# Kernel optimization log

Hardware: AMD Instinct MI355X
Metric: run time of the kernel (lower is better)

Reference implementation:

```python
import jax, jax.numpy as jnp
import numpy as np

N = 6000          # num nodes (max_nodes)
E = 192000        # num edges
NTYPES = 100
NCLUST = 4        # hardcoded num_nodes=4 in diff_pool_net.__init__
OUT = 16
BN_EPS = 1e-5

PARAM_SHAPES = {
    'emb_w': (NTYPES, 64),
    # gnn1_pool: GNN(64, 64, 4, lin=True); DenseSAGEConv: lin_rel (no bias) + lin_root (bias)
    'pw1r': (64, 64), 'pw1l': (64, 64), 'pb1': (64,),
    'pw2r': (64, 64), 'pw2l': (64, 64), 'pb2': (64,),
    'pw3r': (NCLUST, 64), 'pw3l': (NCLUST, 64), 'pb3': (NCLUST,),
    'plin_w': (NCLUST, 2 * 64 + NCLUST), 'plin_b': (NCLUST,),
    # gnn1_embed: GNN(64, 64, 64, lin=False)
    'ew1r': (64, 64), 'ew1l': (64, 64), 'eb1': (64,),
    'ew2r': (64, 64), 'ew2l': (64, 64), 'eb2': (64,),
    'ew3r': (64, 64), 'ew3l': (64, 64), 'eb3': (64,),
    'lin1_w': (64, 192), 'lin1_b': (64,),
    'lin2_w': (OUT, 64), 'lin2_b': (OUT,),
    'embl_w': (32, 192), 'embl_b': (32,),
    'lin3_w': (OUT, 32 + OUT), 'lin3_b': (OUT,),
}


def _lin(x, w, b=None):
    y = x @ w.T
    return y if b is None else y + b


def _sage(x, adj, wr, wl, b):
    # DenseSAGEConv: mean-aggregate over dense adj, then lin_rel(agg) + lin_root(x)
    agg = jnp.matmul(adj, x)
    deg = jnp.clip(jnp.sum(adj, axis=-1, keepdims=True), 1.0, None)
    return _lin(agg / deg, wr) + _lin(x, wl, b)


def _bn(x):
    # training-mode BatchNorm1d with default gamma=1, beta=0 (biased variance)
    c = x.shape[-1]
    xf = x.reshape(-1, c)
    m = jnp.mean(xf, axis=0)
    v = jnp.var(xf, axis=0)
    return ((xf - m) * jax.lax.rsqrt(v + BN_EPS)).reshape(x.shape)


def _gnn(x, adj, wr1, wl1, b1, wr2, wl2, b2, wr3, wl3, b3, lw=None, lb=None):
    x1 = _bn(jax.nn.relu(_sage(x, adj, wr1, wl1, b1)))
    x2 = _bn(jax.nn.relu(_sage(x1, adj, wr2, wl2, b2)))
    x3 = _bn(jax.nn.relu(_sage(x2, adj, wr3, wl3, b3)))
    xc = jnp.concatenate([x1, x2, x3], axis=-1)
    if lw is not None:
        xc = jax.nn.relu(_lin(xc, lw, lb))
    return xc


def _forward(p, edge_index, node_types):
    # to_dense_adj: scatter-add edges into a dense [1, N, N] adjacency
    adj = jnp.zeros((N, N), jnp.float32).at[edge_index[0], edge_index[1]].add(1.0)[None]
    x = p['emb_w'][node_types][None]                      # [1, N, 64]
    s = _gnn(x, adj, p['pw1r'], p['pw1l'], p['pb1'],
             p['pw2r'], p['pw2l'], p['pb2'],
             p['pw3r'], p['pw3l'], p['pb3'],
             p['plin_w'], p['plin_b'])                    # [1, N, 4]
    xe = _gnn(x, adj, p['ew1r'], p['ew1l'], p['eb1'],
              p['ew2r'], p['ew2l'], p['eb2'],
              p['ew3r'], p['ew3l'], p['eb3'])             # [1, N, 192]
    x_embed = _lin(xe, p['embl_w'], p['embl_b'])          # [1, N, 32]
    # dense_diff_pool pooled features: softmax(S)^T @ X (pooled adj/losses are unused downstream)
    ssm = jax.nn.softmax(s, axis=-1)
    s_x = jnp.einsum('bnk,bnc->bkc', ssm, xe)             # [1, 4, 192]
    s_x = jax.nn.relu(_lin(s_x, p['lin1_w'], p['lin1_b']))
    s_x = _lin(s_x, p['lin2_w'], p['lin2_b'])             # [1, 4, OUT]
    # one_hot=True branch: per-node gather of its cluster row (vectorized form of the python loop)
    idx = jnp.argmax(s, axis=-1)                          # [1, N]
    res = jnp.take(s_x[0], idx[0], axis=0)[None]          # [1, N, OUT]
    return _lin(jnp.concatenate([x_embed, res], axis=-1), p['lin3_w'], p['lin3_b'])


def setup_inputs() -> dict:
    key = jax.random.key(0)
    ks = jax.random.split(key, len(PARAM_SHAPES) + 2)
    inp = {n: jax.random.normal(k, shp, jnp.float32) * 0.1
           for (n, shp), k in zip(PARAM_SHAPES.items(), ks)}
    inp['edge_index'] = jax.random.randint(ks[-2], (2, E), 0, N)
    inp['node_types'] = jax.random.randint(ks[-1], (N,), 0, NTYPES)
    return inp


def reference(edge_index, node_types, emb_w, pw1r, pw1l, pb1, pw2r, pw2l, pb2,
              pw3r, pw3l, pb3, plin_w, plin_b, ew1r, ew1l, eb1, ew2r, ew2l, eb2,
              ew3r, ew3l, eb3, lin1_w, lin1_b, lin2_w, lin2_b, embl_w, embl_b,
              lin3_w, lin3_b):
    args = locals()
    p = {k: args[k] for k in PARAM_SHAPES}
    return _forward(p, edge_index, node_types)
```

## Files before the change

kernel.cpp:

```cpp
#include <hip/hip_runtime.h>
#include <hip/hip_bf16.h>

#define NN 6000
#define EE 192000

#define W_DEG     0
#define W_CUR     6000
#define W_STATS   12000
#define W_SXACC   12768
#define W_ZEND    13536
#define W_FLAG    13536
#define W_ROWPTR  13540
#define W_COL     19544
#define W_X0      211544
#define W_ZP1     595544
#define W_ZP2     979544
#define W_ZP3     1363544
#define W_ZE1     1387544
#define W_ZE2     1771544
#define W_ZE3     2155544
#define W_S       2539544
#define W_SX2     2563544
#define W_PAR     2563608

struct PtrTab {
  const void* src[29];
  int off[29];
  int cnt[29];
};

__device__ __forceinline__ float bf2f(unsigned short h) {
  return __uint_as_float(((unsigned)h) << 16);
}
__device__ __forceinline__ int rfl(int x) { return __builtin_amdgcn_readfirstlane(x); }

__global__ void k_detect(const void* emb, int* flag) {
  __shared__ int bad;
  if (threadIdx.x == 0) bad = 0;
  __syncthreads();
  const unsigned short* p = (const unsigned short*)emb;
  float v0 = bf2f(p[threadIdx.x]);
  float v1 = bf2f(p[threadIdx.x + 256]);
  if (!(fabsf(v0) <= 100.f) || !(fabsf(v1) <= 100.f)) bad = 1;
  __syncthreads();
  if (threadIdx.x == 0) flag[0] = bad ? 0 : 1;
}

__global__ void k_convert(PtrTab tab, float* base, const int* flag) {
  int b = blockIdx.x;
  const void* s = tab.src[b];
  float* d = base + tab.off[b];
  int n = tab.cnt[b];
  bool bf = (flag[0] == 1);
  if (bf) {
    const unsigned short* sp = (const unsigned short*)s;
    for (int i = threadIdx.x; i < n; i += 256) d[i] = bf2f(sp[i]);
  } else {
    const float* sp = (const float*)s;
    for (int i = threadIdx.x; i < n; i += 256) d[i] = sp[i];
  }
}

__global__ void k_deg(const int* __restrict__ ei, int* __restrict__ deg) {
  int e = blockIdx.x * 256 + threadIdx.x;
  if (e < EE) atomicAdd(&deg[ei[e]], 1);
}

__global__ void k_scan(const int* __restrict__ deg, int* __restrict__ rowptr) {
  __shared__ int part[1024];
  int t = threadIdx.x;
  int base = t * 6;
  int loc[6]; int s = 0;
#pragma unroll
  for (int j = 0; j < 6; ++j) { int i = base + j; int v = (i < NN) ? deg[i] : 0; loc[j] = s; s += v; }
  part[t] = s;
  __syncthreads();
  for (int off = 1; off < 1024; off <<= 1) {
    int v = part[t];
    int add = (t >= off) ? part[t - off] : 0;
    __syncthreads();
    part[t] = v + add;
    __syncthreads();
  }
  int pre = (t == 0) ? 0 : part[t - 1];
#pragma unroll
  for (int j = 0; j < 6; ++j) { int i = base + j; if (i <= NN) rowptr[i] = pre + loc[j]; }
}

__global__ void k_scatter(const int* __restrict__ ei, const int* __restrict__ rowptr,
                          int* __restrict__ cur, int* __restrict__ col) {
  int e = blockIdx.x * 256 + threadIdx.x;
  if (e < EE) {
    int s = ei[e], d = ei[EE + e];
    int pos = atomicAdd(&cur[s], 1);
    col[rowptr[s] + pos] = d;
  }
}

__global__ void k_emb(const float* __restrict__ emb, const int* __restrict__ nt, float* __restrict__ x0) {
  int t = blockIdx.x * 256 + threadIdx.x;
  int i = t >> 4, q = t & 15;
  *(float4*)&x0[i * 64 + q * 4] = *(const float4*)&emb[nt[i] * 64 + q * 4];
}

template <int OUT, bool HS>
__device__ __forceinline__ void sage_body(
    const float* __restrict__ in_z, const float* __restrict__ in_stats,
    const float* __restrict__ wr, const float* __restrict__ wl, const float* __restrict__ bias,
    const int* __restrict__ rowptr, const int* __restrict__ col,
    float* __restrict__ out_z, float* __restrict__ out_stats,
    int vb, int total_waves,
    float* __restrict__ wrT, float* __restrict__ wlT, float* __restrict__ bs,
    float (* __restrict__ vec)[2][64], float (* __restrict__ red)[2][64]) {
  int tid = threadIdx.x, lane = tid & 63, wv = tid >> 6;

  for (int i = tid; i < 64 * OUT; i += 256) {
    int f = i >> 6, k = i & 63;
    wrT[k * (OUT + 1) + f] = wr[i];
    wlT[k * (OUT + 1) + f] = wl[i];
  }
  if (tid < OUT) bs[tid] = bias[tid];

  float m = 0.f, r = 1.f;
  if (HS) {
    float s = in_stats[lane], q = in_stats[64 + lane];
    m = s * (1.f / NN);
    r = rsqrtf(q * (1.f / NN) - m * m + 1e-5f);
  }
  __syncthreads();

  float accs = 0.f, accq = 0.f;
  int ol = lane & (OUT - 1);
  int wave_id = vb * 4 + wv;
  for (int n = wave_id; n < NN; n += total_waves) {
    float x = (in_z[n * 64 + lane] - m) * r;
    int rs = rfl(rowptr[n]), re = rfl(rowptr[n + 1]);
    int cnt = re - rs;
    float sz = 0.f;
    for (int base = rs; base < re; base += 64) {
      int ci = base + lane;
      int colv = col[ci < re ? ci : (re - 1)];
      int full = re - base; if (full > 64) full = 64;
      int ng8 = (full + 7) >> 3;
      for (int g = 0; g < ng8; ++g) {
        int e0 = g * 8;
#pragma unroll
        for (int u = 0; u < 8; ++u) {
          int j = __builtin_amdgcn_readlane(colv, e0 + u);
          float v = in_z[j * 64 + lane];
          sz += (e0 + u < full) ? v : 0.f;
        }
      }
    }
    float fc = (float)cnt;
    float inv = 1.f / (float)(cnt > 0 ? cnt : 1);
    float a = (sz - fc * m) * r * inv;
    vec[wv][0][lane] = a;
    vec[wv][1][lane] = x;
    float y = bs[ol];
    const float* va = &vec[wv][0][0];
    const float* vx = &vec[wv][1][0];
#pragma unroll
    for (int kk = 0; kk < 16; ++kk) {
      const float4 a4 = *(const float4*)(va + kk * 4);
      const float4 x4 = *(const float4*)(vx + kk * 4);
      int k0 = kk * 4;
      y += a4.x * wrT[(k0 + 0) * (OUT + 1) + ol] + x4.x * wlT[(k0 + 0) * (OUT + 1) + ol];
      y += a4.y * wrT[(k0 + 1) * (OUT + 1) + ol] + x4.y * wlT[(k0 + 1) * (OUT + 1) + ol];
      y += a4.z * wrT[(k0 + 2) * (OUT + 1) + ol] + x4.z * wlT[(k0 + 2) * (OUT + 1) + ol];
      y += a4.w * wrT[(k0 + 3) * (OUT + 1) + ol] + x4.w * wlT[(k0 + 3) * (OUT + 1) + ol];
    }
    float z = fmaxf(y, 0.f);
    if (lane < OUT) {
      out_z[n * OUT + lane] = z;
      accs += z; accq += z * z;
    }
  }
  if (lane < OUT) { red[wv][0][lane] = accs; red[wv][1][lane] = accq; }
  __syncthreads();
  if (tid < OUT) {
    float s = red[0][0][tid] + red[1][0][tid] + red[2][0][tid] + red[3][0][tid];
    float q = red[0][1][tid] + red[1][1][tid] + red[2][1][tid] + red[3][1][tid];
    atomicAdd(&out_stats[tid], s);
    atomicAdd(&out_stats[64 + tid], q);
  }
}

template <int OUTA, int OUTB, bool HS>
__global__ __launch_bounds__(256, 4) void k_dual(
    const float* __restrict__ inA, const float* __restrict__ stA,
    const float* __restrict__ wrA, const float* __restrict__ wlA, const float* __restrict__ bA,
    float* __restrict__ outA, float* __restrict__ ostA,
    const float* __restrict__ inB, const float* __restrict__ stB,
    const float* __restrict__ wrB, const float* __restrict__ wlB, const float* __restrict__ bB,
    float* __restrict__ outB, float* __restrict__ ostB,
    const int* __restrict__ rowptr, const int* __restrict__ col, int G) {
  __shared__ float wrT[64 * 65];
  __shared__ float wlT[64 * 65];
  __shared__ float bs[64];
  __shared__ float vec[4][2][64];
  __shared__ float red[4][2][64];
  int bx = (int)blockIdx.x;
  int hi = (bx >> 2) & 1;
  int vb = (bx >> 3) * 4 + (bx & 3);
  if (hi == 0)
    sage_body<OUTA, HS>(inA, stA, wrA, wlA, bA, rowptr, col, outA, ostA,
                        vb, G * 4, wrT, wlT, bs, vec, red);
  else
    sage_body<OUTB, HS>(inB, stB, wrB, wlB, bB, rowptr, col, outB, ostB,
                        vb, G * 4, wrT, wlT, bs, vec, red);
}

__global__ __launch_bounds__(256) void k_pool(
    const float* __restrict__ zp1, const float* __restrict__ zp2, const float* __restrict__ zp3,
    const float* __restrict__ sp1, const float* __restrict__ sp2, const float* __restrict__ sp3,
    const float* __restrict__ ze1, const float* __restrict__ ze2, const float* __restrict__ ze3,
    const float* __restrict__ se1, const float* __restrict__ se2, const float* __restrict__ se3,
    const float* __restrict__ plw, const float* __restrict__ plb,
    float* __restrict__ s_out, float* __restrict__ sx_acc) {
  __shared__ float red[4][12][64];
  int tid = threadIdx.x, lane = tid & 63, wv = tid >> 6;

  float mp1 = sp1[lane] * (1.f / NN); float rp1 = rsqrtf(sp1[64 + lane] * (1.f / NN) - mp1 * mp1 + 1e-5f);
  float mp2 = sp2[lane] * (1.f / NN); float rp2 = rsqrtf(sp2[64 + lane] * (1.f / NN) - mp2 * mp2 + 1e-5f);
  float mp3 = 0.f, rp3 = 1.f;
  if (lane < 4) { mp3 = sp3[lane] * (1.f / NN); rp3 = rsqrtf(sp3[64 + lane] * (1.f / NN) - mp3 * mp3 + 1e-5f); }
  float me1 = se1[lane] * (1.f / NN); float re1 = rsqrtf(se1[64 + lane] * (1.f / NN) - me1 * me1 + 1e-5f);
  float me2 = se2[lane] * (1.f / NN); float re2 = rsqrtf(se2[64 + lane] * (1.f / NN) - me2 * me2 + 1e-5f);
  float me3 = se3[lane] * (1.f / NN); float re3 = rsqrtf(se3[64 + lane] * (1.f / NN) - me3 * me3 + 1e-5f);

  float w0a = plw[0 * 132 + lane], w0b = plw[0 * 132 + 64 + lane], w0c = (lane < 4) ? plw[0 * 132 + 128 + lane] : 0.f;
  float w1a = plw[1 * 132 + lane], w1b = plw[1 * 132 + 64 + lane], w1c = (lane < 4) ? plw[1 * 132 + 128 + lane] : 0.f;
  float w2a = plw[2 * 132 + lane], w2b = plw[2 * 132 + 64 + lane], w2c = (lane < 4) ? plw[2 * 132 + 128 + lane] : 0.f;
  float w3a = plw[3 * 132 + lane], w3b = plw[3 * 132 + 64 + lane], w3c = (lane < 4) ? plw[3 * 132 + 128 + lane] : 0.f;
  float pb0 = plb[0], pb1v = plb[1], pb2v = plb[2], pb3v = plb[3];

  float acc[12];
#pragma unroll
  for (int u = 0; u < 12; ++u) acc[u] = 0.f;

  int wave_id = blockIdx.x * 4 + wv;
  for (int n = wave_id; n < NN; n += 1500) {
    float a = (zp1[n * 64 + lane] - mp1) * rp1;
    float b = (zp2[n * 64 + lane] - mp2) * rp2;
    float c = (lane < 4) ? ((zp3[n * 4 + lane] - mp3) * rp3) : 0.f;
    float p0 = a * w0a + b * w0b + c * w0c;
    float p1 = a * w1a + b * w1b + c * w1c;
    float p2 = a * w2a + b * w2b + c * w2c;
    float p3 = a * w3a + b * w3b + c * w3c;
#pragma unroll
    for (int off = 1; off < 64; off <<= 1) {
      p0 += __shfl_xor(p0, off);
      p1 += __shfl_xor(p1, off);
      p2 += __shfl_xor(p2, off);
      p3 += __shfl_xor(p3, off);
    }
    float s0 = fmaxf(p0 + pb0, 0.f), s1 = fmaxf(p1 + pb1v, 0.f);
    float s2 = fmaxf(p2 + pb2v, 0.f), s3 = fmaxf(p3 + pb3v, 0.f);
    if (lane < 4) {
      float sv = (lane == 0) ? s0 : (lane == 1) ? s1 : (lane == 2) ? s2 : s3;
      s_out[n * 4 + lane] = sv;
    }
    float mx = fmaxf(fmaxf(s0, s1), fmaxf(s2, s3));
    float e0 = __expf(s0 - mx), e1 = __expf(s1 - mx), e2 = __expf(s2 - mx), e3 = __expf(s3 - mx);
    float inv = 1.f / (e0 + e1 + e2 + e3);
    e0 *= inv; e1 *= inv; e2 *= inv; e3 *= inv;
    float x1 = (ze1[n * 64 + lane] - me1) * re1;
    float x2 = (ze2[n * 64 + lane] - me2) * re2;
    float x3 = (ze3[n * 64 + lane] - me3) * re3;
    acc[0] += e0 * x1; acc[1] += e0 * x2; acc[2] += e0 * x3;
    acc[3] += e1 * x1; acc[4] += e1 * x2; acc[5] += e1 * x3;
    acc[6] += e2 * x1; acc[7] += e2 * x2; acc[8] += e2 * x3;
    acc[9] += e3 * x1; acc[10] += e3 * x2; acc[11] += e3 * x3;
  }
#pragma unroll
  for (int u = 0; u < 12; ++u) red[wv][u][lane] = acc[u];
  __syncthreads();
  for (int u = tid; u < 768; u += 256) {
    int f = u & 63, q = u >> 6;
    float v = red[0][q][f] + red[1][q][f] + red[2][q][f] + red[3][q][f];
    int k = q / 3, slot = q - 3 * k;
    atomicAdd(&sx_acc[k * 192 + slot * 64 + f], v);
  }
}

__global__ void k_mlp(const float* __restrict__ sx, const float* __restrict__ l1w, const float* __restrict__ l1b,
                      const float* __restrict__ l2w, const float* __restrict__ l2b, float* __restrict__ sx2) {
  __shared__ float tl[4][64];
  int tid = threadIdx.x;
  int k = tid >> 6, f = tid & 63;
  float v = l1b[f];
  for (int c = 0; c < 192; ++c) v += sx[k * 192 + c] * l1w[f * 192 + c];
  tl[k][f] = fmaxf(v, 0.f);
  __syncthreads();
  if (tid < 64) {
    int kk = tid >> 4, o = tid & 15;
    float u = l2b[o];
#pragma unroll
    for (int j = 0; j < 64; ++j) u += tl[kk][j] * l2w[o * 64 + j];
    sx2[kk * 16 + o] = u;
  }
}

__global__ __launch_bounds__(256) void k_final(
    const float* __restrict__ ze1, const float* __restrict__ ze2, const float* __restrict__ ze3,
    const float* __restrict__ se1, const float* __restrict__ se2, const float* __restrict__ se3,
    const float* __restrict__ ew, const float* __restrict__ ebv,
    const float* __restrict__ l3w, const float* __restrict__ l3b,
    const float* __restrict__ s_out, const float* __restrict__ sx2,
    const int* __restrict__ flag, void* __restrict__ out) {
  __shared__ float ewT[192 * 33];
  __shared__ float l3T[48 * 17];
  __shared__ float ebs[32], l3bs[16];
  __shared__ float xev[4][192];
  __shared__ float xed[4][32];
  int tid = threadIdx.x, lane = tid & 63, wv = tid >> 6;

  for (int i = tid; i < 6144; i += 256) { int cp = i / 192, c = i - cp * 192; ewT[c * 33 + cp] = ew[i]; }
  for (int i = tid; i < 768; i += 256) { int o = i / 48, j = i - o * 48; l3T[j * 17 + o] = l3w[i]; }
  if (tid < 32) ebs[tid] = ebv[tid];
  if (tid < 16) l3bs[tid] = l3b[tid];

  float me1 = se1[lane] * (1.f / NN); float re1 = rsqrtf(se1[64 + lane] * (1.f / NN) - me1 * me1 + 1e-5f);
  float me2 = se2[lane] * (1.f / NN); float re2 = rsqrtf(se2[64 + lane] * (1.f / NN) - me2 * me2 + 1e-5f);
  float me3 = se3[lane] * (1.f / NN); float re3 = rsqrtf(se3[64 + lane] * (1.f / NN) - me3 * me3 + 1e-5f);
  bool bf = (flag[0] == 1);
  __syncthreads();

  int h = lane >> 5, L = lane & 31;
  int wave_id = blockIdx.x * 4 + wv;
  for (int n = wave_id; n < NN; n += 2048) {
    float x1 = (ze1[n * 64 + lane] - me1) * re1;
    float x2 = (ze2[n * 64 + lane] - me2) * re2;
    float x3 = (ze3[n * 64 + lane] - me3) * re3;
    xev[wv][lane] = x1;
    xev[wv][64 + lane] = x2;
    xev[wv][128 + lane] = x3;
    float v = (h == 0) ? ebs[L] : 0.f;
    int cb = h * 96;
#pragma unroll
    for (int c4 = 0; c4 < 24; ++c4) {
      const float4 xv = *(const float4*)&xev[wv][cb + c4 * 4];
      int c0 = cb + c4 * 4;
      v += xv.x * ewT[(c0 + 0) * 33 + L];
      v += xv.y * ewT[(c0 + 1) * 33 + L];
      v += xv.z * ewT[(c0 + 2) * 33 + L];
      v += xv.w * ewT[(c0 + 3) * 33 + L];
    }
    v += __shfl_xor(v, 32);
    if (h == 0) xed[wv][L] = v;
    if (lane < 16) {
      int idx = 0; float best = s_out[n * 4 + 0];
      float c1 = s_out[n * 4 + 1]; if (c1 > best) { best = c1; idx = 1; }
      float c2 = s_out[n * 4 + 2]; if (c2 > best) { best = c2; idx = 2; }
      float c3 = s_out[n * 4 + 3]; if (c3 > best) { best = c3; idx = 3; }
      float racc = l3bs[lane];
#pragma unroll
      for (int j = 0; j < 32; ++j) racc += xed[wv][j] * l3T[j * 17 + lane];
      const float* sxr = sx2 + idx * 16;
#pragma unroll
      for (int j = 0; j < 16; ++j) racc += sxr[j] * l3T[(32 + j) * 17 + lane];
      if (bf) ((__hip_bfloat16*)out)[n * 16 + lane] = __float2bfloat16(racc);
      else    ((float*)out)[n * 16 + lane] = racc;
    }
  }
}

extern "C" void kernel_launch(void* const* d_in, const int* in_sizes, int n_in,
                              void* d_out, int out_size, void* d_ws, size_t ws_size,
                              hipStream_t stream) {
  float* F = (float*)d_ws;
  int* I = (int*)d_ws;

  static const int pcnt[29] = {6400, 4096, 4096, 64, 4096, 4096, 64, 256, 256, 4, 528, 4,
                               4096, 4096, 64, 4096, 4096, 64, 4096, 4096, 64,
                               12288, 64, 1024, 16, 6144, 32, 768, 16};
  int poff[29];
  { int a = 0; for (int i = 0; i < 29; ++i) { poff[i] = a; a += pcnt[i]; } }

  PtrTab tab;
  for (int i = 0; i < 29; ++i) { tab.src[i] = d_in[i]; tab.off[i] = poff[i]; tab.cnt[i] = pcnt[i]; }

  const int* ei = (const int*)d_in[29];
  const int* nt = (const int*)d_in[30];

  int* deg = I + W_DEG;
  int* cur = I + W_CUR;
  int* rowptr = I + W_ROWPTR;
  int* col = I + W_COL;
  int* flag = I + W_FLAG;
  float* st = F + W_STATS;
  float* sxacc = F + W_SXACC;
  float* x0 = F + W_X0;
  float* zp1 = F + W_ZP1; float* zp2 = F + W_ZP2; float* zp3 = F + W_ZP3;
  float* ze1 = F + W_ZE1; float* ze2 = F + W_ZE2; float* ze3 = F + W_ZE3;
  float* sbuf = F + W_S;
  float* sx2 = F + W_SX2;
  float* P = F + W_PAR;
#define PP(i) (P + poff[i])

  hipMemsetAsync(d_ws, 0, (size_t)W_ZEND * 4, stream);
  k_detect<<<1, 256, 0, stream>>>(d_in[0], flag);
  k_convert<<<29, 256, 0, stream>>>(tab, P, flag);
  k_deg<<<750, 256, 0, stream>>>(ei, deg);
  k_scan<<<1, 1024, 0, stream>>>(deg, rowptr);
  k_scatter<<<750, 256, 0, stream>>>(ei, rowptr, cur, col);
  k_emb<<<375, 256, 0, stream>>>(PP(0), nt, x0);

  k_dual<64, 64, false><<<1024, 256, 0, stream>>>(
      x0, nullptr, PP(1), PP(2), PP(3), zp1, st + 0 * 128,
      x0, nullptr, PP(12), PP(13), PP(14), ze1, st + 3 * 128,
      rowptr, col, 512);
  k_dual<64, 64, true><<<1024, 256, 0, stream>>>(
      zp1, st + 0 * 128, PP(4), PP(5), PP(6), zp2, st + 1 * 128,
      ze1, st + 3 * 128, PP(15), PP(16), PP(17), ze2, st + 4 * 128,
      rowptr, col, 512);
  k_dual<4, 64, true><<<1024, 256, 0, stream>>>(
      zp2, st + 1 * 128, PP(7), PP(8), PP(9), zp3, st + 2 * 128,
      ze2, st + 4 * 128, PP(18), PP(19), PP(20), ze3, st + 5 * 128,
      rowptr, col, 512);

  k_pool<<<375, 256, 0, stream>>>(zp1, zp2, zp3, st + 0 * 128, st + 1 * 128, st + 2 * 128,
                                  ze1, ze2, ze3, st + 3 * 128, st + 4 * 128, st + 5 * 128,
                                  PP(10), PP(11), sbuf, sxacc);
  k_mlp<<<1, 256, 0, stream>>>(sxacc, PP(21), PP(22), PP(23), PP(24), sx2);
  k_final<<<512, 256, 0, stream>>>(ze1, ze2, ze3, st + 3 * 128, st + 4 * 128, st + 5 * 128,
                                   PP(25), PP(26), PP(27), PP(28), sbuf, sx2, flag, d_out);
}
```

Measured before the change: 291.6 us.

## Fuse prelude kernels, fold MLP into final kernel, process two nodes per wave in SAGE

Merges the dtype-detect, parameter-convert, embedding-gather and degree-count kernels into one prelude launch, with every block redoing the cheap detection itself. Folds the tiny cluster MLP into each block of the final kernel so it no longer runs as a separate single-block launch. Changes the SAGE aggregation so each wave handles two nodes at once, interleaving their neighbor gathers to expose more memory-level parallelism. The trade-offs are the MLP being recomputed redundantly in every final block, higher register pressure, and wasted lanes when the two nodes' degrees differ.

```diff
diff --git a/kernel.cpp b/kernel.cpp
--- a/kernel.cpp
+++ b/kernel.cpp
@@ -34,36 +34,50 @@
 }
 __device__ __forceinline__ int rfl(int x) { return __builtin_amdgcn_readfirstlane(x); }
 
-__global__ void k_detect(const void* emb, int* flag) {
-  __shared__ int bad;
-  if (threadIdx.x == 0) bad = 0;
-  __syncthreads();
-  const unsigned short* p = (const unsigned short*)emb;
-  float v0 = bf2f(p[threadIdx.x]);
-  float v1 = bf2f(p[threadIdx.x + 256]);
-  if (!(fabsf(v0) <= 100.f) || !(fabsf(v1) <= 100.f)) bad = 1;
-  __syncthreads();
-  if (threadIdx.x == 0) flag[0] = bad ? 0 : 1;
-}
-
-__global__ void k_convert(PtrTab tab, float* base, const int* flag) {
+__global__ __launch_bounds__(256) void k_prelude(
+    PtrTab tab, float* __restrict__ base,
+    const int* __restrict__ nt, float* __restrict__ x0,
+    const int* __restrict__ ei, int* __restrict__ deg, int* __restrict__ flag) {
+  __shared__ int s_ok;
+  int tid = threadIdx.x;
+  const unsigned short* ep = (const unsigned short*)tab.src[0];
+  if (tid == 0) s_ok = 1;
+  __syncthreads();
+  float v0 = bf2f(ep[tid]), v1 = bf2f(ep[tid + 256]);
+  if (!(fabsf(v0) <= 100.f) || !(fabsf(v1) <= 100.f)) atomicAnd(&s_ok, 0);
+  __syncthreads();
+  bool bf = (s_ok != 0);
   int b = blockIdx.x;
-  const void* s = tab.src[b];
-  float* d = base + tab.off[b];
-  int n = tab.cnt[b];
-  bool bf = (flag[0] == 1);
-  if (bf) {
-    const unsigned short* sp = (const unsigned short*)s;
-    for (int i = threadIdx.x; i < n; i += 256) d[i] = bf2f(sp[i]);
+  if (b == 0 && tid == 0) flag[0] = bf ? 1 : 0;
+
+  if (b < 29) {
+    const void* s = tab.src[b];
+    float* d = base + tab.off[b];
+    int n = tab.cnt[b];
+    if (bf) {
+      const unsigned short* sp = (const unsigned short*)s;
+      for (int i = tid; i < n; i += 256) d[i] = bf2f(sp[i]);
+    } else {
+      const float* sp = (const float*)s;
+      for (int i = tid; i < n; i += 256) d[i] = sp[i];
+    }
+  } else if (b < 404) {
+    int t = (b - 29) * 256 + tid;
+    int i = t >> 4, q = t & 15;
+    int row = nt[i];
+    if (bf) {
+      const unsigned short* sp = (const unsigned short*)tab.src[0] + row * 64 + q * 4;
+      float4 o;
+      o.x = bf2f(sp[0]); o.y = bf2f(sp[1]); o.z = bf2f(sp[2]); o.w = bf2f(sp[3]);
+      *(float4*)&x0[i * 64 + q * 4] = o;
+    } else {
+      *(float4*)&x0[i * 64 + q * 4] =
+          *(const float4*)((const float*)tab.src[0] + row * 64 + q * 4);
+    }
   } else {
-    const float* sp = (const float*)s;
-    for (int i = threadIdx.x; i < n; i += 256) d[i] = sp[i];
-  }
-}
-
-__global__ void k_deg(const int* __restrict__ ei, int* __restrict__ deg) {
-  int e = blockIdx.x * 256 + threadIdx.x;
-  if (e < EE) atomicAdd(&deg[ei[e]], 1);
+    int e = (b - 404) * 256 + tid;
+    if (e < EE) atomicAdd(&deg[ei[e]], 1);
+  }
 }
 
 __global__ void k_scan(const int* __restrict__ deg, int* __restrict__ rowptr) {
@@ -95,12 +109,6 @@
     int pos = atomicAdd(&cur[s], 1);
     col[rowptr[s] + pos] = d;
   }
-}
-
-__global__ void k_emb(const float* __restrict__ emb, const int* __restrict__ nt, float* __restrict__ x0) {
-  int t = blockIdx.x * 256 + threadIdx.x;
-  int i = t >> 4, q = t & 15;
-  *(float4*)&x0[i * 64 + q * 4] = *(const float4*)&emb[nt[i] * 64 + q * 4];
 }
 
 template <int OUT, bool HS>
@@ -111,7 +119,7 @@
     float* __restrict__ out_z, float* __restrict__ out_stats,
     int vb, int total_waves,
     float* __restrict__ wrT, float* __restrict__ wlT, float* __restrict__ bs,
-    float (* __restrict__ vec)[2][64], float (* __restrict__ red)[2][64]) {
+    float (* __restrict__ vec)[4][64], float (* __restrict__ red)[2][64]) {
   int tid = threadIdx.x, lane = tid & 63, wv = tid >> 6;
 
   for (int i = tid; i < 64 * OUT; i += 256) {
@@ -132,48 +140,78 @@
   float accs = 0.f, accq = 0.f;
   int ol = lane & (OUT - 1);
   int wave_id = vb * 4 + wv;
-  for (int n = wave_id; n < NN; n += total_waves) {
-    float x = (in_z[n * 64 + lane] - m) * r;
-    int rs = rfl(rowptr[n]), re = rfl(rowptr[n + 1]);
-    int cnt = re - rs;
-    float sz = 0.f;
-    for (int base = rs; base < re; base += 64) {
-      int ci = base + lane;
-      int colv = col[ci < re ? ci : (re - 1)];
-      int full = re - base; if (full > 64) full = 64;
-      int ng8 = (full + 7) >> 3;
+  int stride2 = 2 * total_waves;
+  for (int n0 = wave_id; n0 < NN; n0 += stride2) {
+    int n1 = n0 + total_waves;
+    bool has1 = n1 < NN;
+    float x0v = (in_z[n0 * 64 + lane] - m) * r;
+    float x1v = has1 ? (in_z[n1 * 64 + lane] - m) * r : 0.f;
+    int rs0 = rfl(rowptr[n0]), re0 = rfl(rowptr[n0 + 1]);
+    int rs1 = rs0, re1 = rs0;
+    if (has1) { rs1 = rfl(rowptr[n1]); re1 = rfl(rowptr[n1 + 1]); }
+    int cnt0 = re0 - rs0, cnt1 = re1 - rs1;
+    float sz0 = 0.f, sz1 = 0.f;
+    int it0 = (cnt0 + 63) >> 6, it1 = (cnt1 + 63) >> 6;
+    int iters = it0 > it1 ? it0 : it1;
+    for (int c = 0; c < iters; ++c) {
+      int b0 = rs0 + (c << 6), b1 = rs1 + (c << 6);
+      int ci0 = b0 + lane, ci1 = b1 + lane;
+      int colv0 = col[(c < it0 && ci0 < re0) ? ci0 : 0];
+      int colv1 = col[(c < it1 && ci1 < re1) ? ci1 : 0];
+      int full0 = re0 - b0; full0 = full0 < 0 ? 0 : (full0 > 64 ? 64 : full0);
+      int full1 = re1 - b1; full1 = full1 < 0 ? 0 : (full1 > 64 ? 64 : full1);
+      int fm = full0 > full1 ? full0 : full1;
+      int ng8 = (fm + 7) >> 3;
       for (int g = 0; g < ng8; ++g) {
         int e0 = g * 8;
 #pragma unroll
         for (int u = 0; u < 8; ++u) {
-          int j = __builtin_amdgcn_readlane(colv, e0 + u);
-          float v = in_z[j * 64 + lane];
-          sz += (e0 + u < full) ? v : 0.f;
+          int j0 = __builtin_amdgcn_readlane(colv0, e0 + u);
+          int j1 = __builtin_amdgcn_readlane(colv1, e0 + u);
+          float v0 = in_z[j0 * 64 + lane];
+          float v1 = in_z[j1 * 64 + lane];
+          sz0 += (e0 + u < full0) ? v0 : 0.f;
+          sz1 += (e0 + u < full1) ? v1 : 0.f;
         }
       }
     }
-    float fc = (float)cnt;
-    float inv = 1.f / (float)(cnt > 0 ? cnt : 1);
-    float a = (sz - fc * m) * r * inv;
-    vec[wv][0][lane] = a;
-    vec[wv][1][lane] = x;
-    float y = bs[ol];
-    const float* va = &vec[wv][0][0];
-    const float* vx = &vec[wv][1][0];
+    float fc0 = (float)cnt0, inv0 = 1.f / (float)(cnt0 > 0 ? cnt0 : 1);
+    float fc1 = (float)cnt1, inv1 = 1.f / (float)(cnt1 > 0 ? cnt1 : 1);
+    float a0 = (sz0 - fc0 * m) * r * inv0;
+    float a1 = (sz1 - fc1 * m) * r * inv1;
+    vec[wv][0][lane] = a0;
+    vec[wv][1][lane] = x0v;
+    vec[wv][2][lane] = a1;
+    vec[wv][3][lane] = x1v;
+    float y0 = bs[ol], y1 = y0;
+    const float* va0 = &vec[wv][0][0];
+    const float* vx0 = &vec[wv][1][0];
+    const float* va1 = &vec[wv][2][0];
+    const float* vx1 = &vec[wv][3][0];
 #pragma unroll
     for (int kk = 0; kk < 16; ++kk) {
-      const float4 a4 = *(const float4*)(va + kk * 4);
-      const float4 x4 = *(const float4*)(vx + kk * 4);
+      const float4 A0 = *(const float4*)(va0 + kk * 4);
+      const float4 X0 = *(const float4*)(vx0 + kk * 4);
+      const float4 A1 = *(const float4*)(va1 + kk * 4);
+      const float4 X1 = *(const float4*)(vx1 + kk * 4);
       int k0 = kk * 4;
-      y += a4.x * wrT[(k0 + 0) * (OUT + 1) + ol] + x4.x * wlT[(k0 + 0) * (OUT + 1) + ol];
-      y += a4.y * wrT[(k0 + 1) * (OUT + 1) + ol] + x4.y * wlT[(k0 + 1) * (OUT + 1) + ol];
-      y += a4.z * wrT[(k0 + 2) * (OUT + 1) + ol] + x4.z * wlT[(k0 + 2) * (OUT + 1) + ol];
-      y += a4.w * wrT[(k0 + 3) * (OUT + 1) + ol] + x4.w * wlT[(k0 + 3) * (OUT + 1) + ol];
-    }
-    float z = fmaxf(y, 0.f);
+      float w_r0 = wrT[(k0 + 0) * (OUT + 1) + ol], w_l0 = wlT[(k0 + 0) * (OUT + 1) + ol];
+      float w_r1 = wrT[(k0 + 1) * (OUT + 1) + ol], w_l1 = wlT[(k0 + 1) * (OUT + 1) + ol];
+      float w_r2 = wrT[(k0 + 2) * (OUT + 1) + ol], w_l2 = wlT[(k0 + 2) * (OUT + 1) + ol];
+      float w_r3 = wrT[(k0 + 3) * (OUT + 1) + ol], w_l3 = wlT[(k0 + 3) * (OUT + 1) + ol];
+      y0 += A0.x * w_r0 + X0.x * w_l0;  y1 += A1.x * w_r0 + X1.x * w_l0;
+      y0 += A0.y * w_r1 + X0.y * w_l1;  y1 += A1.y * w_r1 + X1.y * w_l1;
+      y0 += A0.z * w_r2 + X0.z * w_l2;  y1 += A1.z * w_r2 + X1.z * w_l2;
+      y0 += A0.w * w_r3 + X0.w * w_l3;  y1 += A1.w * w_r3 + X1.w * w_l3;
+    }
+    float z0 = fmaxf(y0, 0.f), z1 = fmaxf(y1, 0.f);
     if (lane < OUT) {
-      out_z[n * OUT + lane] = z;
-      accs += z; accq += z * z;
+      out_z[n0 * OUT + lane] = z0;
+      accs += z0; accq += z0 * z0;
+      if (has1) {
+        out_z[n1 * OUT + lane] = z1;
+        accs += z1; accq += z1 * z1;
+      }
     }
   }
   if (lane < OUT) { red[wv][0][lane] = accs; red[wv][1][lane] = accq; }
@@ -198,7 +236,7 @@
   __shared__ float wrT[64 * 65];
   __shared__ float wlT[64 * 65];
   __shared__ float bs[64];
-  __shared__ float vec[4][2][64];
+  __shared__ float vec[4][4][64];
   __shared__ float red[4][2][64];
   int bx = (int)blockIdx.x;
   int hi = (bx >> 2) & 1;
@@ -284,42 +322,50 @@
   }
 }
 
-__global__ void k_mlp(const float* __restrict__ sx, const float* __restrict__ l1w, const float* __restrict__ l1b,
-                      const float* __restrict__ l2w, const float* __restrict__ l2b, float* __restrict__ sx2) {
-  __shared__ float tl[4][64];
-  int tid = threadIdx.x;
-  int k = tid >> 6, f = tid & 63;
-  float v = l1b[f];
-  for (int c = 0; c < 192; ++c) v += sx[k * 192 + c] * l1w[f * 192 + c];
-  tl[k][f] = fmaxf(v, 0.f);
-  __syncthreads();
-  if (tid < 64) {
-    int kk = tid >> 4, o = tid & 15;
-    float u = l2b[o];
-#pragma unroll
-    for (int j = 0; j < 64; ++j) u += tl[kk][j] * l2w[o * 64 + j];
-    sx2[kk * 16 + o] = u;
-  }
-}
-
 __global__ __launch_bounds__(256) void k_final(
     const float* __restrict__ ze1, const float* __restrict__ ze2, const float* __restrict__ ze3,
     const float* __restrict__ se1, const float* __restrict__ se2, const float* __restrict__ se3,
     const float* __restrict__ ew, const float* __restrict__ ebv,
     const float* __restrict__ l3w, const float* __restrict__ l3b,
-    const float* __restrict__ s_out, const float* __restrict__ sx2,
+    const float* __restrict__ s_out,
+    const float* __restrict__ sxacc,
+    const float* __restrict__ l1w, const float* __restrict__ l1b,
+    const float* __restrict__ l2w, const float* __restrict__ l2b,
     const int* __restrict__ flag, void* __restrict__ out) {
   __shared__ float ewT[192 * 33];
   __shared__ float l3T[48 * 17];
   __shared__ float ebs[32], l3bs[16];
   __shared__ float xev[4][192];
   __shared__ float xed[4][32];
+  __shared__ float tl[4][64];
+  __shared__ float sx2l[64];
   int tid = threadIdx.x, lane = tid & 63, wv = tid >> 6;
 
   for (int i = tid; i < 6144; i += 256) { int cp = i / 192, c = i - cp * 192; ewT[c * 33 + cp] = ew[i]; }
   for (int i = tid; i < 768; i += 256) { int o = i / 48, j = i - o * 48; l3T[j * 17 + o] = l3w[i]; }
   if (tid < 32) ebs[tid] = ebv[tid];
   if (tid < 16) l3bs[tid] = l3b[tid];
+
+  {
+    int k = tid >> 6, f = tid & 63;
+    float v = l1b[f];
+    const float4* Ar = (const float4*)(sxacc + k * 192);
+    const float4* Wr = (const float4*)(l1w + f * 192);
+#pragma unroll 8
+    for (int c4 = 0; c4 < 48; ++c4) {
+      float4 a = Ar[c4], w = Wr[c4];
+      v += a.x * w.x + a.y * w.y + a.z * w.z + a.w * w.w;
+    }
+    tl[k][f] = fmaxf(v, 0.f);
+  }
+  __syncthreads();
+  if (tid < 64) {
+    int kk = tid >> 4, o = tid & 15;
+    float u = l2b[o];
+#pragma unroll
+    for (int j = 0; j < 64; ++j) u += tl[kk][j] * l2w[o * 64 + j];
+    sx2l[kk * 16 + o] = u;
+  }
 
   float me1 = se1[lane] * (1.f / NN); float re1 = rsqrtf(se1[64 + lane] * (1.f / NN) - me1 * me1 + 1e-5f);
   float me2 = se2[lane] * (1.f / NN); float re2 = rsqrtf(se2[64 + lane] * (1.f / NN) - me2 * me2 + 1e-5f);
@@ -357,7 +403,7 @@
       float racc = l3bs[lane];
 #pragma unroll
       for (int j = 0; j < 32; ++j) racc += xed[wv][j] * l3T[j * 17 + lane];
-      const float* sxr = sx2 + idx * 16;
+      const float* sxr = sx2l + idx * 16;
 #pragma unroll
       for (int j = 0; j < 16; ++j) racc += sxr[j] * l3T[(32 + j) * 17 + lane];
       if (bf) ((__hip_bfloat16*)out)[n * 16 + lane] = __float2bfloat16(racc);
@@ -395,17 +441,13 @@
   float* zp1 = F + W_ZP1; float* zp2 = F + W_ZP2; float* zp3 = F + W_ZP3;
   float* ze1 = F + W_ZE1; float* ze2 = F + W_ZE2; float* ze3 = F + W_ZE3;
   float* sbuf = F + W_S;
-  float* sx2 = F + W_SX2;
   float* P = F + W_PAR;
 #define PP(i) (P + poff[i])
 
   hipMemsetAsync(d_ws, 0, (size_t)W_ZEND * 4, stream);
-  k_detect<<<1, 256, 0, stream>>>(d_in[0], flag);
-  k_convert<<<29, 256, 0, stream>>>(tab, P, flag);
-  k_deg<<<750, 256, 0, stream>>>(ei, deg);
+  k_prelude<<<1154, 256, 0, stream>>>(tab, P, nt, x0, ei, deg, flag);
   k_scan<<<1, 1024, 0, stream>>>(deg, rowptr);
   k_scatter<<<750, 256, 0, stream>>>(ei, rowptr, cur, col);
-  k_emb<<<375, 256, 0, stream>>>(PP(0), nt, x0);
 
   k_dual<64, 64, false><<<1024, 256, 0, stream>>>(
       x0, nullptr, PP(1), PP(2), PP(3), zp1, st + 0 * 128,
@@ -423,7 +465,7 @@
   k_pool<<<375, 256, 0, stream>>>(zp1, zp2, zp3, st + 0 * 128, st + 1 * 128, st + 2 * 128,
                                   ze1, ze2, ze3, st + 3 * 128, st + 4 * 128, st + 5 * 128,
                                   PP(10), PP(11), sbuf, sxacc);
-  k_mlp<<<1, 256, 0, stream>>>(sxacc, PP(21), PP(22), PP(23), PP(24), sx2);
   k_final<<<512, 256, 0, stream>>>(ze1, ze2, ze3, st + 3 * 128, st + 4 * 128, st + 5 * 128,
-                                   PP(25), PP(26), PP(27), PP(28), sbuf, sx2, flag, d_out);
-}
+                                   PP(25), PP(26), PP(27), PP(28), sbuf,
+                                   sxacc, PP(21), PP(22), PP(23), PP(24), flag, d_out);
+}
```

Result: slower. 306.7 us (+5.2%).
